# Optimization experiments

Measured on AMD Instinct MI355X. Metric: run time of the kernel, lower is better.

Reference implementation:

```python
import jax, jax.numpy as jnp
import numpy as np

N_INPUTS = 128
N_LATENT = 21
LEN_TIME = 51
NUM_SHIFTS = 50
BATCH = 2048
N_HIDDEN = 4  # hidden relu layers in the outer DenseResBlock


def setup_inputs() -> dict:
    key = jax.random.key(0)
    ks = jax.random.split(key, 8)
    s = 0.05  # small init scale keeps activations sane through the residual stack
    return {
        "inputs": jax.random.normal(ks[0], (BATCH, LEN_TIME, N_INPUTS), jnp.float32),
        "L": jnp.eye(N_LATENT, dtype=jnp.float32)
             + s * jax.random.normal(ks[1], (N_LATENT, N_LATENT), jnp.float32),
        "ienc_W": s * jax.random.normal(ks[2], (N_INPUTS, N_LATENT), jnp.float32),
        "idec_W": s * jax.random.normal(ks[3], (N_LATENT, N_INPUTS), jnp.float32),
        "enc_W": s * jax.random.normal(ks[4], (N_HIDDEN, N_INPUTS, N_INPUTS), jnp.float32),
        "enc_b": jnp.zeros((N_HIDDEN, N_INPUTS), jnp.float32),
        "enc_Wo": s * jax.random.normal(ks[5], (N_INPUTS, N_INPUTS), jnp.float32),
        "enc_bo": jnp.zeros((N_INPUTS,), jnp.float32),
        "dec_W": s * jax.random.normal(ks[6], (N_HIDDEN, N_INPUTS, N_INPUTS), jnp.float32),
        "dec_b": jnp.zeros((N_HIDDEN, N_INPUTS), jnp.float32),
        "dec_Wo": s * jax.random.normal(ks[7], (N_INPUTS, N_INPUTS), jnp.float32),
        "dec_bo": jnp.zeros((N_INPUTS,), jnp.float32),
    }


def _resblock(x, W, b, Wo, bo):
    # DenseResBlock: stack of relu Dense layers + linear output + residual skip.
    h = x
    for i in range(W.shape[0]):  # fixed small layer count
        h = jax.nn.relu(h @ W[i] + b[i])
    return x + h @ Wo + bo


def reference(inputs, L, ienc_W, idec_W, enc_W, enc_b, enc_Wo, enc_bo,
              dec_W, dec_b, dec_Wo, dec_bo):
    B, T, n_in = inputs.shape
    len_pred = T - NUM_SHIFTS  # = 1

    auto_in = inputs.reshape(-1, n_in)                        # [B*T, n_in]
    pred_in = inputs[:, :len_pred, :].reshape(-1, n_in)       # [B*len_pred, n_in]

    # autoencoder path
    pe = _resblock(auto_in, enc_W, enc_b, enc_Wo, enc_bo)     # partially encoded
    fe = pe @ ienc_W                                          # fully encoded [., n_latent]
    pd = fe @ idec_W                                          # partially decoded
    autoencoder_output = _resblock(pd, dec_W, dec_b, dec_Wo, dec_bo)
    outer_auto_output = _resblock(pe, dec_W, dec_b, dec_Wo, dec_bo)

    # latent rollout: z_{k+1} = z_k @ L, decode every step
    pe_pred = _resblock(pred_in, enc_W, enc_b, enc_Wo, enc_bo)
    z0 = pe_pred @ ienc_W                                     # [B*len_pred, n_latent]

    def step(z, _):
        z_next = z @ L
        return z_next, z_next

    _, zs = jax.lax.scan(step, z0, None, length=NUM_SHIFTS)   # [S, B*len_pred, n_latent]

    # decode all shifts in one large batched pass (same math as per-shift decode)
    dec_in = zs.reshape(-1, zs.shape[-1]) @ idec_W            # [S*B*len_pred, n_in]
    dec_all = _resblock(dec_in, dec_W, dec_b, dec_Wo, dec_bo)
    predictions = (dec_all
                   .reshape(NUM_SHIFTS, B, len_pred, n_in)
                   .transpose(1, 0, 2, 3)
                   .reshape(B, NUM_SHIFTS * len_pred, n_in))

    return autoencoder_output, outer_auto_output, predictions
```

## Files before the change

### kernel.cpp

```cpp
#include <hip/hip_runtime.h>

#define NF 128
#define NLAT 21
#define NBATCH 2048
#define LEN_T 51
#define NSHIFT 50
#define AUTO_ROWS (NBATCH*LEN_T)
#define PRED_ROWS (NBATCH*NSHIFT)

typedef short bh8  __attribute__((ext_vector_type(8)));
typedef unsigned short us8 __attribute__((ext_vector_type(8)));
typedef float f32x4  __attribute__((ext_vector_type(4)));
typedef float f32x16 __attribute__((ext_vector_type(16)));

#define MFMA32(A,B,C) __builtin_amdgcn_mfma_f32_32x32x16_bf16(A,B,C,0,0,0)
#define SGB(m,n) __builtin_amdgcn_sched_group_barrier((m),(n),0)

__device__ __forceinline__ float bf2f(short s){
  unsigned u = ((unsigned)(unsigned short)s) << 16;
  return __builtin_bit_cast(float, u);
}
__device__ __forceinline__ short f2bf(float v){
  unsigned u = __builtin_bit_cast(unsigned, v);
  return (short)((u + 0x7FFFu + ((u>>16)&1u)) >> 16);
}

__global__ void k_mmul(const float* __restrict__ ienc, const float* __restrict__ idec,
                       float* __restrict__ M){
  int idx = blockIdx.x*256 + threadIdx.x;
  int i = idx>>7, j = idx&127;
  float s = 0.f;
#pragma unroll
  for(int k=0;k<NLAT;++k) s = fmaf(ienc[i*NLAT+k], idec[k*NF+j], s);
  M[idx] = s;
}

__global__ void k_prep(const float* __restrict__ encW, const float* __restrict__ encWo,
                       const float* __restrict__ decW, const float* __restrict__ decWo,
                       const float* __restrict__ M,    const float* __restrict__ idec,
                       unsigned short* __restrict__ swz){
  int id  = blockIdx.x*256 + threadIdx.x;
  int mat = id >> 11;
  int rem = id & 2047;
  int f   = rem >> 6, l = rem & 63;
  int s   = f >> 2,  mt = f & 3;
  int hl  = l >> 5,  c  = l & 31;
  const float* src;
  if(mat<4)       src = encW + mat*16384;
  else if(mat==4) src = encWo;
  else if(mat<9)  src = decW + (mat-5)*16384;
  else if(mat==9) src = decWo;
  else if(mat==10)src = M;
  else            src = idec;
  us8 w8;
#pragma unroll
  for(int i=0;i<8;++i){
    int k = s*16 + 4*hl + (i&3) + 8*(i>>2);
    float v;
    if(mat==11) v = (k<NLAT) ? src[k*NF + mt*32 + c] : 0.f;
    else        v = src[k*NF + mt*32 + c];
    w8[i] = (unsigned short)f2bf(v);
  }
  *(us8*)(swz + (size_t)mat*16384 + (size_t)f*512 + (size_t)l*8) = w8;
}

__device__ __forceinline__ void stage_w(const unsigned short* __restrict__ g,
                                        unsigned short* l, int tid){
  __syncthreads();
#pragma unroll
  for(int i=0;i<8;++i)
    *(us8*)(l + i*2048 + tid*8) = *(const us8*)(g + i*2048 + tid*8);
  __syncthreads();
}

__device__ __forceinline__ void ldw4(const unsigned short* wl, int s, int lane, bh8 w[4]){
#pragma unroll
  for(int mt=0;mt<4;++mt) w[mt] = *(const bh8*)(wl + (s*4+mt)*512 + lane*8);
}
__device__ __forceinline__ void mm4(const bh8 w[4], bh8 b, f32x16 acc[4]){
#pragma unroll
  for(int mt=0;mt<4;++mt) acc[mt]=MFMA32(w[mt],b,acc[mt]);
}
__device__ __forceinline__ void run_layer(const unsigned short* wl,
    const bh8 h[8], f32x16 acc[4], int lane){
#pragma unroll
  for(int mt=0;mt<4;++mt){
    f32x16 z;
#pragma unroll
    for(int r=0;r<16;++r) z[r]=0.f;
    acc[mt]=z;
  }
  bh8 wA[4], wB[4];
  ldw4(wl,0,lane,wA);   SGB(0x100,4);
  ldw4(wl,1,lane,wB);   SGB(0x100,4);
  mm4(wA,h[0],acc);     SGB(0x8,4);
  ldw4(wl,2,lane,wA);   SGB(0x100,4);
  mm4(wB,h[1],acc);     SGB(0x8,4);
  ldw4(wl,3,lane,wB);   SGB(0x100,4);
  mm4(wA,h[2],acc);     SGB(0x8,4);
  ldw4(wl,4,lane,wA);   SGB(0x100,4);
  mm4(wB,h[3],acc);     SGB(0x8,4);
  ldw4(wl,5,lane,wB);   SGB(0x100,4);
  mm4(wA,h[4],acc);     SGB(0x8,4);
  ldw4(wl,6,lane,wA);   SGB(0x100,4);
  mm4(wB,h[5],acc);     SGB(0x8,4);
  ldw4(wl,7,lane,wB);   SGB(0x100,4);
  mm4(wA,h[6],acc);     SGB(0x8,4);
  mm4(wB,h[7],acc);     SGB(0x8,4);
}

__device__ __forceinline__ void epi_hidden(f32x16 acc[4], const float* __restrict__ bias,
    bh8 h[8], int hl){
#pragma unroll
  for(int mt=0;mt<4;++mt){
    f32x16 a = acc[mt];
#pragma unroll
    for(int q=0;q<4;++q){
      f32x4 b = *(const f32x4*)(bias + mt*32 + q*8 + hl*4);
#pragma unroll
      for(int j=0;j<4;++j) a[q*4+j]+=b[j];
    }
#pragma unroll
    for(int r=0;r<16;++r) a[r]=fmaxf(a[r],0.f);
#pragma unroll
    for(int p=0;p<2;++p){
      bh8 o;
#pragma unroll
      for(int i=0;i<8;++i) o[i]=f2bf(a[p*8 + (i>>2)*4 + (i&3)]);
      h[mt*2+p]=o;
    }
  }
}
__device__ __forceinline__ void epi_plain(f32x16 acc[4], bh8 h[8], int hl){
#pragma unroll
  for(int mt=0;mt<4;++mt){
    f32x16 a = acc[mt];
#pragma unroll
    for(int p=0;p<2;++p){
      bh8 o;
#pragma unroll
      for(int i=0;i<8;++i) o[i]=f2bf(a[p*8 + (i>>2)*4 + (i&3)]);
      h[mt*2+p]=o;
    }
  }
}

__device__ __forceinline__ void frag_store(unsigned short* fb, int s, const bh8& v, int lane){
  *(bh8*)(fb + s*512 + lane*8) = v;
}
__device__ __forceinline__ bh8 frag_load(const unsigned short* fb, int s, int lane){
  return *(const bh8*)(fb + s*512 + lane*8);
}

__device__ __forceinline__ void final_direct(float* __restrict__ rowptr,
    f32x16 acc[4], const float* __restrict__ bo,
    const unsigned short* fb, int lane, int hl){
#pragma unroll
  for(int mt=0;mt<4;++mt){
    f32x16 a = acc[mt];
#pragma unroll
    for(int q=0;q<4;++q){
      f32x4 b = *(const f32x4*)(bo + mt*32 + q*8 + hl*4);
#pragma unroll
      for(int j=0;j<4;++j) a[q*4+j]+=b[j];
    }
    bh8 r0 = frag_load(fb, 2*mt,   lane);
    bh8 r1 = frag_load(fb, 2*mt+1, lane);
#pragma unroll
    for(int r=0;r<16;++r){
      int i=((r>>2)&1)*4+(r&3);
      a[r] += bf2f(r<8 ? r0[i] : r1[i]);
    }
#pragma unroll
    for(int q=0;q<4;++q){
      f32x4 w; w[0]=a[q*4+0]; w[1]=a[q*4+1]; w[2]=a[q*4+2]; w[3]=a[q*4+3];
      *(f32x4*)(rowptr + mt*32 + q*8 + hl*4) = w;
    }
  }
}

__device__ __forceinline__ void dec_block(const unsigned short* __restrict__ swz,
    unsigned short* wlds, const float* __restrict__ decB,
    bh8 h[8], f32x16 acc[4], int tid, int lane, int hl){
#pragma unroll 1
  for(int l=0;l<4;++l){
    stage_w(swz + (size_t)(5+l)*16384, wlds, tid);
    run_layer(wlds, h, acc, lane);
    epi_hidden(acc, decB + l*NF, h, hl);
  }
  stage_w(swz + (size_t)9*16384, wlds, tid);
  run_layer(wlds, h, acc, lane);
}

__global__ __launch_bounds__(256,2)
void k_main2(const float* __restrict__ gin, const unsigned short* __restrict__ swz,
             const float* __restrict__ encB, const float* __restrict__ encBo,
             const float* __restrict__ decB, const float* __restrict__ decBo,
             float* __restrict__ out1, float* __restrict__ out2, float* __restrict__ pe0){
  __shared__ unsigned short wlds[16384];
  __shared__ unsigned short fragbuf[16384];
  const int tid=threadIdx.x, lane=tid&63, wid=tid>>6;
  const int hl=lane>>5, c31=lane&31;
  const int grow0=blockIdx.x*128;
  const int myrow=grow0 + wid*32 + c31;
  unsigned short* fb = fragbuf + wid*4096;
  bh8 h[8];
  f32x16 acc[4];

#pragma unroll
  for(int s=0;s<8;++s){
    f32x4 a=*(const f32x4*)(gin + (size_t)myrow*NF + s*16 + 4*hl);
    f32x4 b=*(const f32x4*)(gin + (size_t)myrow*NF + s*16 + 8 + 4*hl);
    bh8 o;
#pragma unroll
    for(int i=0;i<4;++i){ o[i]=f2bf(a[i]); o[i+4]=f2bf(b[i]); }
    h[s]=o;
    frag_store(fb, s, o, lane);
  }

#pragma unroll 1
  for(int l=0;l<4;++l){
    stage_w(swz + (size_t)l*16384, wlds, tid);
    run_layer(wlds, h, acc, lane);
    epi_hidden(acc, encB + l*NF, h, hl);
  }
  stage_w(swz + (size_t)4*16384, wlds, tid);
  run_layer(wlds, h, acc, lane);

  {
    int bidx = myrow / LEN_T;
    bool isz = (myrow == bidx*LEN_T);
#pragma unroll
    for(int mt=0;mt<4;++mt){
      f32x16 a = acc[mt];
#pragma unroll
      for(int q=0;q<4;++q){
        f32x4 b = *(const f32x4*)(encBo + mt*32 + q*8 + hl*4);
#pragma unroll
        for(int j=0;j<4;++j) a[q*4+j]+=b[j];
      }
      bh8 r0 = frag_load(fb, 2*mt,   lane);
      bh8 r1 = frag_load(fb, 2*mt+1, lane);
#pragma unroll
      for(int r=0;r<16;++r){
        int i=((r>>2)&1)*4+(r&3);
        a[r] += bf2f(r<8 ? r0[i] : r1[i]);
      }
      if(isz){
#pragma unroll
        for(int q=0;q<4;++q){
          f32x4 w; w[0]=a[q*4+0]; w[1]=a[q*4+1]; w[2]=a[q*4+2]; w[3]=a[q*4+3];
          *(f32x4*)(pe0 + (size_t)bidx*NF + mt*32 + q*8 + hl*4) = w;
        }
      }
#pragma unroll
      for(int p=0;p<2;++p){
        bh8 o;
#pragma unroll
        for(int i=0;i<8;++i) o[i]=f2bf(a[p*8 + (i>>2)*4 + (i&3)]);
        h[mt*2+p]=o;
      }
    }
#pragma unroll
    for(int s=0;s<8;++s) frag_store(fb, s, h[s], lane);
  }

  dec_block(swz, wlds, decB, h, acc, tid, lane, hl);
  final_direct(out2 + (size_t)myrow*NF, acc, decBo, fb, lane, hl);

#pragma unroll
  for(int s=0;s<8;++s) h[s]=frag_load(fb, s, lane);
  stage_w(swz + (size_t)10*16384, wlds, tid);
  run_layer(wlds, h, acc, lane);
  epi_plain(acc, h, hl);
#pragma unroll
  for(int s=0;s<8;++s) frag_store(fb, s, h[s], lane);

  dec_block(swz, wlds, decB, h, acc, tid, lane, hl);
  final_direct(out1 + (size_t)myrow*NF, acc, decBo, fb, lane, hl);
}

__global__ void k_roll(const float* __restrict__ pe0, const float* __restrict__ ienc,
                       const float* __restrict__ L, float* __restrict__ zs){
  const int tid=threadIdx.x, lane=tid&63, wid=tid>>6, sub=lane&31, half=lane>>5;
  const int row=blockIdx.x*8 + wid*2 + half;
  const bool act = sub < NLAT;
  float Lc[NLAT];
#pragma unroll
  for(int k=0;k<NLAT;++k) Lc[k] = act ? L[k*NLAT+sub] : 0.f;
  float z=0.f;
  if(act){
    const float* pr = pe0 + (size_t)row*NF;
    float s0=0.f,s1=0.f,s2=0.f,s3=0.f;
#pragma unroll 8
    for(int k=0;k<NF;k+=4){
      s0=fmaf(pr[k+0], ienc[(k+0)*NLAT+sub], s0);
      s1=fmaf(pr[k+1], ienc[(k+1)*NLAT+sub], s1);
      s2=fmaf(pr[k+2], ienc[(k+2)*NLAT+sub], s2);
      s3=fmaf(pr[k+3], ienc[(k+3)*NLAT+sub], s3);
    }
    z=(s0+s1)+(s2+s3);
  }
  const int base = half*32;
#pragma unroll 1
  for(int s=0;s<NSHIFT;++s){
    float zn=0.f;
#pragma unroll
    for(int k=0;k<NLAT;++k) zn=fmaf(__shfl(z, base+k, 64), Lc[k], zn);
    z=zn;
    if(act) zs[((size_t)s*NBATCH + row)*NLAT + sub] = z;
  }
}

__global__ __launch_bounds__(256,2)
void k_pred2(const float* __restrict__ zs, const unsigned short* __restrict__ swz,
             const float* __restrict__ decB, const float* __restrict__ decBo,
             float* __restrict__ out3){
  __shared__ unsigned short wlds[16384];
  __shared__ unsigned short fragbuf[16384];
  const int tid=threadIdx.x, lane=tid&63, wid=tid>>6;
  const int hl=lane>>5, c31=lane&31;
  const int grow0=blockIdx.x*128;
  const int prow=grow0 + wid*32 + c31;
  unsigned short* fb = fragbuf + wid*4096;
  bh8 h[8];
  f32x16 acc[4];

  bh8 zf[2];
  {
    const float* zr = zs + (size_t)prow*NLAT;
#pragma unroll
    for(int s=0;s<2;++s){
      bh8 o;
#pragma unroll
      for(int i=0;i<8;++i){
        int cc = s*16 + 4*hl + (i&3) + 8*(i>>2);
        o[i] = (cc<NLAT) ? f2bf(zr[cc]) : (short)0;
      }
      zf[s]=o;
    }
  }
  stage_w(swz + (size_t)11*16384, wlds, tid);
  {
#pragma unroll
    for(int mt=0;mt<4;++mt){
      f32x16 z;
#pragma unroll
      for(int r=0;r<16;++r) z[r]=0.f;
      acc[mt]=z;
    }
    bh8 wA[4], wB[4];
    ldw4(wlds,0,lane,wA);  SGB(0x100,4);
    ldw4(wlds,1,lane,wB);  SGB(0x100,4);
    mm4(wA,zf[0],acc);     SGB(0x8,4);
    mm4(wB,zf[1],acc);     SGB(0x8,4);
  }
  epi_plain(acc, h, hl);
#pragma unroll
  for(int s=0;s<8;++s) frag_store(fb, s, h[s], lane);

  dec_block(swz, wlds, decB, h, acc, tid, lane, hl);

  int sh = prow >> 11, b = prow & 2047;
  final_direct(out3 + ((size_t)b*NSHIFT + sh)*NF, acc, decBo, fb, lane, hl);
}

extern "C" void kernel_launch(void* const* d_in, const int* in_sizes, int n_in,
                              void* d_out, int out_size, void* d_ws, size_t ws_size,
                              hipStream_t stream) {
  const float* gin   = (const float*)d_in[0];
  const float* L     = (const float*)d_in[1];
  const float* iencW = (const float*)d_in[2];
  const float* idecW = (const float*)d_in[3];
  const float* encW  = (const float*)d_in[4];
  const float* encB  = (const float*)d_in[5];
  const float* encWo = (const float*)d_in[6];
  const float* encBo = (const float*)d_in[7];
  const float* decW  = (const float*)d_in[8];
  const float* decB  = (const float*)d_in[9];
  const float* decWo = (const float*)d_in[10];
  const float* decBo = (const float*)d_in[11];

  float* out1 = (float*)d_out;
  float* out2 = out1 + (size_t)AUTO_ROWS*NF;
  float* out3 = out2 + (size_t)AUTO_ROWS*NF;

  float* M   = (float*)d_ws;
  float* pe0 = M + 16384;
  float* zs  = pe0 + (size_t)NBATCH*NF;
  unsigned short* swz = (unsigned short*)(zs + (size_t)NSHIFT*NBATCH*NLAT);

  hipLaunchKernelGGL(k_mmul, dim3(64),  dim3(256), 0, stream, iencW, idecW, M);
  hipLaunchKernelGGL(k_prep, dim3(96),  dim3(256), 0, stream, encW, encWo, decW, decWo, M, idecW, swz);
  hipLaunchKernelGGL(k_main2, dim3(AUTO_ROWS/128), dim3(256), 0, stream,
                     gin, swz, encB, encBo, decB, decBo, out1, out2, pe0);
  hipLaunchKernelGGL(k_roll, dim3(NBATCH/8), dim3(256), 0, stream, pe0, iencW, L, zs);
  hipLaunchKernelGGL(k_pred2, dim3(PRED_ROWS/128), dim3(256), 0, stream,
                     zs, swz, decB, decBo, out3);
}
```

Before: 179.3 us.

## Double-buffer weight staging with async global-to-LDS loads, keep residuals in registers

Each layer's weights used to be staged into LDS by a blocking copy between two barriers. Now two LDS weight buffers alternate, and the next layer's weights are prefetched with global_load_lds DMA while the current layer's MFMAs run. Residual fragments now stay in registers instead of an LDS scratch buffer, and biases are cached in LDS. The cost is more LDS per block, more VGPRs for the residual copy, and reliance on barrier ordering for the async loads.

```diff
diff --git a/kernel.cpp b/kernel.cpp
--- a/kernel.cpp
+++ b/kernel.cpp
@@ -64,13 +64,16 @@
   *(us8*)(swz + (size_t)mat*16384 + (size_t)f*512 + (size_t)l*8) = w8;
 }
 
-__device__ __forceinline__ void stage_w(const unsigned short* __restrict__ g,
-                                        unsigned short* l, int tid){
-  __syncthreads();
-#pragma unroll
-  for(int i=0;i<8;++i)
-    *(us8*)(l + i*2048 + tid*8) = *(const us8*)(g + i*2048 + tid*8);
-  __syncthreads();
+__device__ __forceinline__ void stage_issue(const unsigned short* g,
+                                            unsigned short* lds, int wid, int lane){
+  const unsigned short* gp = g + wid*512 + lane*8;
+  unsigned short* lp = lds + wid*512;
+#pragma unroll
+  for(int i=0;i<8;++i){
+    __builtin_amdgcn_global_load_lds(
+      (const __attribute__((address_space(1))) void*)(gp + i*2048),
+      (__attribute__((address_space(3))) void*)(lp + i*2048), 16, 0, 0);
+  }
 }
 
 __device__ __forceinline__ void ldw4(const unsigned short* wl, int s, int lane, bh8 w[4]){
@@ -109,7 +112,7 @@
   mm4(wB,h[7],acc);     SGB(0x8,4);
 }
 
-__device__ __forceinline__ void epi_hidden(f32x16 acc[4], const float* __restrict__ bias,
+__device__ __forceinline__ void epi_hidden(f32x16 acc[4], const float* bias,
     bh8 h[8], int hl){
 #pragma unroll
   for(int mt=0;mt<4;++mt){
@@ -145,16 +148,8 @@
   }
 }
 
-__device__ __forceinline__ void frag_store(unsigned short* fb, int s, const bh8& v, int lane){
-  *(bh8*)(fb + s*512 + lane*8) = v;
-}
-__device__ __forceinline__ bh8 frag_load(const unsigned short* fb, int s, int lane){
-  return *(const bh8*)(fb + s*512 + lane*8);
-}
-
 __device__ __forceinline__ void final_direct(float* __restrict__ rowptr,
-    f32x16 acc[4], const float* __restrict__ bo,
-    const unsigned short* fb, int lane, int hl){
+    f32x16 acc[4], const float* bo, const bh8 res[8], int hl){
 #pragma unroll
   for(int mt=0;mt<4;++mt){
     f32x16 a = acc[mt];
@@ -164,8 +159,7 @@
 #pragma unroll
       for(int j=0;j<4;++j) a[q*4+j]+=b[j];
     }
-    bh8 r0 = frag_load(fb, 2*mt,   lane);
-    bh8 r1 = frag_load(fb, 2*mt+1, lane);
+    bh8 r0 = res[2*mt], r1 = res[2*mt+1];
 #pragma unroll
     for(int r=0;r<16;++r){
       int i=((r>>2)&1)*4+(r&3);
@@ -180,16 +174,22 @@
 }
 
 __device__ __forceinline__ void dec_block(const unsigned short* __restrict__ swz,
-    unsigned short* wlds, const float* __restrict__ decB,
-    bh8 h[8], f32x16 acc[4], int tid, int lane, int hl){
+    unsigned short (*wlds)[16384], int& cur, const float* bdec,
+    bh8 h[8], f32x16 acc[4], const unsigned short* next_g,
+    int wid, int lane, int hl){
 #pragma unroll 1
   for(int l=0;l<4;++l){
-    stage_w(swz + (size_t)(5+l)*16384, wlds, tid);
-    run_layer(wlds, h, acc, lane);
-    epi_hidden(acc, decB + l*NF, h, hl);
-  }
-  stage_w(swz + (size_t)9*16384, wlds, tid);
-  run_layer(wlds, h, acc, lane);
+    unsigned short* wc = cur ? wlds[1] : wlds[0];
+    unsigned short* wn = cur ? wlds[0] : wlds[1];
+    stage_issue(swz + (size_t)(l<3 ? 6+l : 9)*16384, wn, wid, lane);
+    run_layer(wc, h, acc, lane);
+    epi_hidden(acc, bdec + l*128, h, hl);
+    __syncthreads(); cur^=1;
+  }
+  unsigned short* wc = cur ? wlds[1] : wlds[0];
+  unsigned short* wn = cur ? wlds[0] : wlds[1];
+  if(next_g) stage_issue(next_g, wn, wid, lane);
+  run_layer(wc, h, acc, lane);
 }
 
 __global__ __launch_bounds__(256,2)
@@ -197,15 +197,19 @@
              const float* __restrict__ encB, const float* __restrict__ encBo,
              const float* __restrict__ decB, const float* __restrict__ decBo,
              float* __restrict__ out1, float* __restrict__ out2, float* __restrict__ pe0){
-  __shared__ unsigned short wlds[16384];
-  __shared__ unsigned short fragbuf[16384];
+  __shared__ __align__(16) unsigned short wlds[2][16384];
+  __shared__ __align__(16) float blds[1280];
   const int tid=threadIdx.x, lane=tid&63, wid=tid>>6;
   const int hl=lane>>5, c31=lane&31;
   const int grow0=blockIdx.x*128;
   const int myrow=grow0 + wid*32 + c31;
-  unsigned short* fb = fragbuf + wid*4096;
-  bh8 h[8];
+  bh8 h[8], res[8];
   f32x16 acc[4];
+
+  stage_issue(swz, wlds[0], wid, lane);
+  for(int i=tid;i<512;i+=256) blds[i]      = encB[i];
+  for(int i=tid;i<512;i+=256) blds[512+i]  = decB[i];
+  if(tid<256) blds[1024+tid] = (tid<128) ? encBo[tid] : decBo[tid-128];
 
 #pragma unroll
   for(int s=0;s<8;++s){
@@ -214,20 +218,25 @@
     bh8 o;
 #pragma unroll
     for(int i=0;i<4;++i){ o[i]=f2bf(a[i]); o[i+4]=f2bf(b[i]); }
-    h[s]=o;
-    frag_store(fb, s, o, lane);
-  }
+    h[s]=o; res[s]=o;
+  }
+  __syncthreads();
+  int cur=0;
 
 #pragma unroll 1
   for(int l=0;l<4;++l){
-    stage_w(swz + (size_t)l*16384, wlds, tid);
-    run_layer(wlds, h, acc, lane);
-    epi_hidden(acc, encB + l*NF, h, hl);
-  }
-  stage_w(swz + (size_t)4*16384, wlds, tid);
-  run_layer(wlds, h, acc, lane);
-
+    unsigned short* wc = cur ? wlds[1] : wlds[0];
+    unsigned short* wn = cur ? wlds[0] : wlds[1];
+    stage_issue(swz + (size_t)(l+1)*16384, wn, wid, lane);
+    run_layer(wc, h, acc, lane);
+    epi_hidden(acc, blds + l*128, h, hl);
+    __syncthreads(); cur^=1;
+  }
   {
+    unsigned short* wc = cur ? wlds[1] : wlds[0];
+    unsigned short* wn = cur ? wlds[0] : wlds[1];
+    stage_issue(swz + (size_t)5*16384, wn, wid, lane);
+    run_layer(wc, h, acc, lane);
     int bidx = myrow / LEN_T;
     bool isz = (myrow == bidx*LEN_T);
 #pragma unroll
@@ -235,12 +244,11 @@
       f32x16 a = acc[mt];
 #pragma unroll
       for(int q=0;q<4;++q){
-        f32x4 b = *(const f32x4*)(encBo + mt*32 + q*8 + hl*4);
+        f32x4 b = *(const f32x4*)(blds + 1024 + mt*32 + q*8 + hl*4);
 #pragma unroll
         for(int j=0;j<4;++j) a[q*4+j]+=b[j];
       }
-      bh8 r0 = frag_load(fb, 2*mt,   lane);
-      bh8 r1 = frag_load(fb, 2*mt+1, lane);
+      bh8 r0=res[2*mt], r1=res[2*mt+1];
 #pragma unroll
       for(int r=0;r<16;++r){
         int i=((r>>2)&1)*4+(r&3);
@@ -262,22 +270,27 @@
       }
     }
 #pragma unroll
-    for(int s=0;s<8;++s) frag_store(fb, s, h[s], lane);
-  }
-
-  dec_block(swz, wlds, decB, h, acc, tid, lane, hl);
-  final_direct(out2 + (size_t)myrow*NF, acc, decBo, fb, lane, hl);
-
-#pragma unroll
-  for(int s=0;s<8;++s) h[s]=frag_load(fb, s, lane);
-  stage_w(swz + (size_t)10*16384, wlds, tid);
-  run_layer(wlds, h, acc, lane);
-  epi_plain(acc, h, hl);
-#pragma unroll
-  for(int s=0;s<8;++s) frag_store(fb, s, h[s], lane);
-
-  dec_block(swz, wlds, decB, h, acc, tid, lane, hl);
-  final_direct(out1 + (size_t)myrow*NF, acc, decBo, fb, lane, hl);
+    for(int s=0;s<8;++s) res[s]=h[s];
+    __syncthreads(); cur^=1;
+  }
+
+  dec_block(swz, wlds, cur, blds+512, h, acc, swz + (size_t)10*16384, wid, lane, hl);
+  final_direct(out2 + (size_t)myrow*NF, acc, blds+1152, res, hl);
+  __syncthreads(); cur^=1;
+
+  {
+    unsigned short* wc = cur ? wlds[1] : wlds[0];
+    unsigned short* wn = cur ? wlds[0] : wlds[1];
+    stage_issue(swz + (size_t)5*16384, wn, wid, lane);
+    run_layer(wc, res, acc, lane);
+    epi_plain(acc, h, hl);
+#pragma unroll
+    for(int s=0;s<8;++s) res[s]=h[s];
+    __syncthreads(); cur^=1;
+  }
+
+  dec_block(swz, wlds, cur, blds+512, h, acc, nullptr, wid, lane, hl);
+  final_direct(out1 + (size_t)myrow*NF, acc, blds+1152, res, hl);
 }
 
 __global__ void k_roll(const float* __restrict__ pe0, const float* __restrict__ ienc,
@@ -316,15 +329,18 @@
 void k_pred2(const float* __restrict__ zs, const unsigned short* __restrict__ swz,
              const float* __restrict__ decB, const float* __restrict__ decBo,
              float* __restrict__ out3){
-  __shared__ unsigned short wlds[16384];
-  __shared__ unsigned short fragbuf[16384];
+  __shared__ __align__(16) unsigned short wlds[2][16384];
+  __shared__ __align__(16) float blds[1280];
   const int tid=threadIdx.x, lane=tid&63, wid=tid>>6;
   const int hl=lane>>5, c31=lane&31;
   const int grow0=blockIdx.x*128;
   const int prow=grow0 + wid*32 + c31;
-  unsigned short* fb = fragbuf + wid*4096;
-  bh8 h[8];
+  bh8 h[8], res[8];
   f32x16 acc[4];
+
+  stage_issue(swz + (size_t)11*16384, wlds[0], wid, lane);
+  for(int i=tid;i<512;i+=256) blds[512+i] = decB[i];
+  if(tid<128) blds[1152+tid] = decBo[tid];
 
   bh8 zf[2];
   {
@@ -340,8 +356,11 @@
       zf[s]=o;
     }
   }
-  stage_w(swz + (size_t)11*16384, wlds, tid);
+  __syncthreads();
+  int cur=0;
+
   {
+    stage_issue(swz + (size_t)5*16384, wlds[1], wid, lane);
 #pragma unroll
     for(int mt=0;mt<4;++mt){
       f32x16 z;
@@ -350,19 +369,20 @@
       acc[mt]=z;
     }
     bh8 wA[4], wB[4];
-    ldw4(wlds,0,lane,wA);  SGB(0x100,4);
-    ldw4(wlds,1,lane,wB);  SGB(0x100,4);
-    mm4(wA,zf[0],acc);     SGB(0x8,4);
-    mm4(wB,zf[1],acc);     SGB(0x8,4);
-  }
-  epi_plain(acc, h, hl);
-#pragma unroll
-  for(int s=0;s<8;++s) frag_store(fb, s, h[s], lane);
-
-  dec_block(swz, wlds, decB, h, acc, tid, lane, hl);
+    ldw4(wlds[0],0,lane,wA);  SGB(0x100,4);
+    ldw4(wlds[0],1,lane,wB);  SGB(0x100,4);
+    mm4(wA,zf[0],acc);        SGB(0x8,4);
+    mm4(wB,zf[1],acc);        SGB(0x8,4);
+    epi_plain(acc, h, hl);
+#pragma unroll
+    for(int s=0;s<8;++s) res[s]=h[s];
+    __syncthreads(); cur^=1;
+  }
+
+  dec_block(swz, wlds, cur, blds+512, h, acc, nullptr, wid, lane, hl);
 
   int sh = prow >> 11, b = prow & 2047;
-  final_direct(out3 + ((size_t)b*NSHIFT + sh)*NF, acc, decBo, fb, lane, hl);
+  final_direct(out3 + ((size_t)b*NSHIFT + sh)*NF, acc, blds+1152, res, hl);
 }
 
 extern "C" void kernel_launch(void* const* d_in, const int* in_sizes, int n_in,
```

Result: faster. 165.6 us (-7.6%).
